# Kernel optimization log

Hardware: AMD Instinct MI355X
Metric: run time of the kernel (lower is better)

The kernel has to match this reference:

```python
import jax, jax.numpy as jnp
import numpy as np

HEADS = 16
EMBED = 1024
HEAD_DIM = EMBED // HEADS


def setup_inputs() -> dict:
    key = jax.random.key(0)
    ks = jax.random.split(key, 7)
    B, S, E = 2, 2048, EMBED
    scale = 1.0 / np.sqrt(E)
    return {
        "query": jax.random.normal(ks[0], (B, S, E), dtype=jnp.float32),
        "key": jax.random.normal(ks[1], (B, S, E), dtype=jnp.float32),
        "value": jax.random.normal(ks[2], (B, S, E), dtype=jnp.float32),
        # nn.Linear(E, E, bias=False) weights, applied as x @ W.T
        "Wq": jax.random.normal(ks[3], (E, E), dtype=jnp.float32) * scale,
        "Wk": jax.random.normal(ks[4], (E, E), dtype=jnp.float32) * scale,
        "Wv": jax.random.normal(ks[5], (E, E), dtype=jnp.float32) * scale,
        "Wo": jax.random.normal(ks[6], (E, E), dtype=jnp.float32) * scale,
    }


def reference(query, key, value, Wq, Wk, Wv, Wo):
    B, S, E = query.shape
    H, D = HEADS, HEAD_DIM

    def split_heads(x, W):
        # [B,S,E] @ W.T -> [B,S,E] -> [B,H,S,D]
        return (x @ W.T).reshape(B, -1, H, D).transpose(0, 2, 1, 3)

    q = split_heads(query, Wq)
    k = split_heads(key, Wk)
    v = split_heads(value, Wv)

    scores = jnp.einsum("bhqd,bhkd->bhqk", q, k) / jnp.sqrt(jnp.float32(D))
    attn = jax.nn.softmax(scores, axis=-1)  # [B,H,S,S]
    x = jnp.einsum("bhqk,bhkd->bhqd", attn, v)
    x = x.transpose(0, 2, 1, 3).reshape(B, -1, H * D)
    return x @ Wo.T
```

## Files before the change

### kernel.cpp

```cpp
#include <hip/hip_runtime.h>
#include <hip/hip_bf16.h>


typedef __attribute__((ext_vector_type(8))) short short8;
typedef __attribute__((ext_vector_type(4))) float f32x4;
typedef __attribute__((ext_vector_type(4))) unsigned short us4;
typedef __attribute__((ext_vector_type(4))) int i32x4;

#define MFMA16(a, b, c) __builtin_amdgcn_mfma_f32_16x16x32_bf16(a, b, c, 0, 0, 0)

static constexpr int B = 2;
static constexpr int S = 2048;
static constexpr int E = 1024;
static constexpr int H = 16;
static constexpr int D = 64;
static constexpr int M = B * S;
static constexpr size_t NE = (size_t)M * E;
static constexpr size_t NW = (size_t)E * E;

static __device__ __forceinline__ unsigned short f2bf(float x) {
  unsigned int u = __float_as_uint(x);
  unsigned int r = (u + 0x7FFFu + ((u >> 16) & 1u)) >> 16;
  return (unsigned short)r;
}

static __device__ __forceinline__ int cvt_pk_bf16(float lo, float hi) {
  int r;
  asm("v_cvt_pk_bf16_f32 %0, %1, %2" : "=v"(r) : "v"(lo), "v"(hi));
  return r;
}

static __device__ __forceinline__ void gload_lds16(const unsigned short* g,
                                                   unsigned short* l) {
  __builtin_amdgcn_global_load_lds(
      (const __attribute__((address_space(1))) unsigned int*)g,
      (__attribute__((address_space(3))) unsigned int*)l, 16, 0, 0);
}

__global__ void cvt_act_kernel(const float* __restrict__ s0,
                               const float* __restrict__ s1,
                               const float* __restrict__ s2,
                               unsigned short* __restrict__ d0,
                               unsigned short* __restrict__ d1,
                               unsigned short* __restrict__ d2, int n4) {
  const float* src = (blockIdx.y == 0) ? s0 : ((blockIdx.y == 1) ? s1 : s2);
  unsigned short* dst = (blockIdx.y == 0) ? d0 : ((blockIdx.y == 1) ? d1 : d2);
  for (int i = blockIdx.x * blockDim.x + threadIdx.x; i < n4;
       i += gridDim.x * blockDim.x) {
    float4 v = reinterpret_cast<const float4*>(src)[i];
    ushort4 o;
    o.x = f2bf(v.x); o.y = f2bf(v.y); o.z = f2bf(v.z); o.w = f2bf(v.w);
    reinterpret_cast<ushort4*>(dst)[i] = o;
  }
}

__global__ void cvt_w_kernel(const float* __restrict__ s0,
                             const float* __restrict__ s1,
                             const float* __restrict__ s2,
                             const float* __restrict__ s3,
                             unsigned short* __restrict__ d0,
                             unsigned short* __restrict__ d1,
                             unsigned short* __restrict__ d2,
                             unsigned short* __restrict__ d3, int n4) {
  const int z = blockIdx.y;
  const float* src = (z == 0) ? s0 : ((z == 1) ? s1 : ((z == 2) ? s2 : s3));
  unsigned short* dst = (z == 0) ? d0 : ((z == 1) ? d1 : ((z == 2) ? d2 : d3));
  for (int i = blockIdx.x * blockDim.x + threadIdx.x; i < n4;
       i += gridDim.x * blockDim.x) {
    float4 v = reinterpret_cast<const float4*>(src)[i];
    ushort4 o;
    o.x = f2bf(v.x); o.y = f2bf(v.y); o.z = f2bf(v.z); o.w = f2bf(v.w);
    reinterpret_cast<ushort4*>(dst)[i] = o;
  }
}

__global__ __launch_bounds__(256) void gemm_proj_kernel(
    const unsigned short* __restrict__ xq, const unsigned short* __restrict__ xk,
    const unsigned short* __restrict__ xv, const unsigned short* __restrict__ wq,
    const unsigned short* __restrict__ wk, const unsigned short* __restrict__ wv,
    unsigned short* __restrict__ Qh, unsigned short* __restrict__ Kh,
    unsigned short* __restrict__ Vt) {
  __shared__ __align__(16) unsigned short As[2][128 * 32];
  __shared__ __align__(16) unsigned short Bs[2][128 * 32];

  const int which = blockIdx.z;
  const unsigned short* A = (which == 0) ? xq : ((which == 1) ? xk : xv);
  const unsigned short* W = (which == 0) ? wq : ((which == 1) ? wk : wv);

  const int wave = threadIdx.x >> 6;
  const int lane = threadIdx.x & 63;
  const int lr = lane & 15;
  const int lk = (lane >> 4) * 8;
  const int m0 = blockIdx.x * 128;
  const int n0 = blockIdx.y * 128;
  const int wm = (wave >> 1) * 64;
  const int wn = (wave & 1) * 64;
  const int srow = lane >> 2;
  const int scol = (lane & 3) * 8;

  f32x4 acc[4][4];
  const f32x4 fz = {0.f, 0.f, 0.f, 0.f};
#pragma unroll
  for (int i = 0; i < 4; ++i)
#pragma unroll
    for (int j = 0; j < 4; ++j) acc[i][j] = fz;

#define STAGE_G(bb, kk)                                                       \
  {                                                                           \
    _Pragma("unroll") for (int i = 0; i < 2; ++i) {                           \
      const int c = wave * 2 + i;                                             \
      const int row = c * 16 + srow;                                          \
      gload_lds16(A + (size_t)(m0 + row) * E + (kk) + scol, &As[bb][c * 512]);\
      gload_lds16(W + (size_t)(n0 + row) * E + (kk) + scol, &Bs[bb][c * 512]);\
    }                                                                         \
  }

  STAGE_G(0, 0);
  __syncthreads();
  int buf = 0;
  for (int kk = 0; kk < E; kk += 32) {
    if (kk + 32 < E) STAGE_G(buf ^ 1, kk + 32);
    short8 af[4], bw[4];
#pragma unroll
    for (int i = 0; i < 4; ++i)
      af[i] = *reinterpret_cast<const short8*>(
          &As[buf][(wm + i * 16 + lr) * 32 + lk]);
#pragma unroll
    for (int j = 0; j < 4; ++j)
      bw[j] = *reinterpret_cast<const short8*>(
          &Bs[buf][(wn + j * 16 + lr) * 32 + lk]);
#pragma unroll
    for (int i = 0; i < 4; ++i)
#pragma unroll
      for (int j = 0; j < 4; ++j) acc[i][j] = MFMA16(af[i], bw[j], acc[i][j]);
    __syncthreads();
    buf ^= 1;
  }
#undef STAGE_G

  const int rbase = (lane >> 4) * 4;
#pragma unroll
  for (int i = 0; i < 4; ++i) {
#pragma unroll
    for (int j = 0; j < 4; ++j) {
      const int col = n0 + wn + j * 16 + lr;
      const int h = col >> 6, d = col & 63;
#pragma unroll
      for (int r = 0; r < 4; ++r) {
        const int row = m0 + wm + i * 16 + rbase + r;
        const int b = row >> 11, s = row & (S - 1);
        const float v = acc[i][j][r];
        if (which == 0) {
          Qh[(((size_t)b * H + h) * S + s) * D + d] = f2bf(v * 0.18033688f);
        } else if (which == 1) {
          Kh[(((size_t)b * H + h) * S + s) * D + d] = f2bf(v);
        } else {
          Vt[(((size_t)b * H + h) * D + d) * S + s] = f2bf(v);
        }
      }
    }
  }
}

__global__ __launch_bounds__(256) void gemm_out_kernel(
    const unsigned short* __restrict__ X, const unsigned short* __restrict__ Wo,
    float* __restrict__ out) {
  __shared__ __align__(16) unsigned short As[2][128 * 32];
  __shared__ __align__(16) unsigned short Bs[2][64 * 32];

  const int wave = threadIdx.x >> 6;
  const int lane = threadIdx.x & 63;
  const int lr = lane & 15;
  const int lk = (lane >> 4) * 8;
  const int m0 = blockIdx.x * 128;
  const int n0 = blockIdx.y * 64;
  const int wm = (wave >> 1) * 64;
  const int wn = (wave & 1) * 32;
  const int srow = lane >> 2;
  const int scol = (lane & 3) * 8;

  f32x4 acc[4][2];
  const f32x4 fz = {0.f, 0.f, 0.f, 0.f};
#pragma unroll
  for (int i = 0; i < 4; ++i)
#pragma unroll
    for (int j = 0; j < 2; ++j) acc[i][j] = fz;

#define STAGE_O(bb, kk)                                                       \
  {                                                                           \
    _Pragma("unroll") for (int i = 0; i < 2; ++i) {                           \
      const int c = wave * 2 + i;                                             \
      const int row = c * 16 + srow;                                          \
      gload_lds16(X + (size_t)(m0 + row) * E + (kk) + scol, &As[bb][c * 512]);\
    }                                                                         \
    gload_lds16(Wo + (size_t)(n0 + wave * 16 + srow) * E + (kk) + scol,       \
                &Bs[bb][wave * 512]);                                         \
  }

  STAGE_O(0, 0);
  __syncthreads();
  int buf = 0;
  for (int kk = 0; kk < E; kk += 32) {
    if (kk + 32 < E) STAGE_O(buf ^ 1, kk + 32);
    short8 af[4], bw[2];
#pragma unroll
    for (int i = 0; i < 4; ++i)
      af[i] = *reinterpret_cast<const short8*>(
          &As[buf][(wm + i * 16 + lr) * 32 + lk]);
#pragma unroll
    for (int j = 0; j < 2; ++j)
      bw[j] = *reinterpret_cast<const short8*>(
          &Bs[buf][(wn + j * 16 + lr) * 32 + lk]);
#pragma unroll
    for (int i = 0; i < 4; ++i)
#pragma unroll
      for (int j = 0; j < 2; ++j) acc[i][j] = MFMA16(af[i], bw[j], acc[i][j]);
    __syncthreads();
    buf ^= 1;
  }
#undef STAGE_O

  const int rbase = (lane >> 4) * 4;
#pragma unroll
  for (int i = 0; i < 4; ++i) {
#pragma unroll
    for (int j = 0; j < 2; ++j) {
      const int col = n0 + wn + j * 16 + lr;
#pragma unroll
      for (int r = 0; r < 4; ++r) {
        const int row = m0 + wm + i * 16 + rbase + r;
        out[(size_t)row * E + col] = acc[i][j][r];
      }
    }
  }
}

__global__ __launch_bounds__(256) void attn_kernel(
    const unsigned short* __restrict__ Qh, const unsigned short* __restrict__ Kh,
    const unsigned short* __restrict__ Vt, unsigned short* __restrict__ Xb) {
  __shared__ __align__(16) unsigned short Ks[2][64 * 64];
  __shared__ __align__(16) unsigned short Vs[2][64 * 64];

  const int wave = threadIdx.x >> 6;
  const int lane = threadIdx.x & 63;
  const int lr = lane & 15;
  const int jj = lane >> 4;
  const int lk = jj * 8;

  const int lin = blockIdx.x + (blockIdx.y << 4);
  const int nlin = (lin & 7) * 64 + (lin >> 3);
  const int qt = nlin & 15;
  const int bh = nlin >> 4;
  const int q0 = qt * 128 + wave * 32;

  const unsigned short* Qp0 = Qh + ((size_t)bh * S + q0) * D;
  const unsigned short* Qp1 = Qp0 + (size_t)16 * D;
  short8 qa0 = *reinterpret_cast<const short8*>(Qp0 + (size_t)lr * D + lk);
  short8 qa1 = *reinterpret_cast<const short8*>(Qp0 + (size_t)lr * D + 32 + lk);
  short8 qb0 = *reinterpret_cast<const short8*>(Qp1 + (size_t)lr * D + lk);
  short8 qb1 = *reinterpret_cast<const short8*>(Qp1 + (size_t)lr * D + 32 + lk);

  const unsigned short* Kbase = Kh + (size_t)bh * S * D;
  const unsigned short* Vbase = Vt + (size_t)bh * D * S;

  const f32x4 fz = {0.f, 0.f, 0.f, 0.f};
  float mrunA = -3.0e38f, lsumA = 0.f;
  float mrunB = -3.0e38f, lsumB = 0.f;
  f32x4 accA[4], accB[4];
#pragma unroll
  for (int dt = 0; dt < 4; ++dt) { accA[dt] = fz; accB[dt] = fz; }

  const int srow = lane >> 3;
  const int sgV = (lane & 7) ^ srow;

#define STAGE_KV(bb, kt)                                                      \
  {                                                                           \
    _Pragma("unroll") for (int i = 0; i < 2; ++i) {                           \
      const int c = wave * 2 + i;                                             \
      const int sgK = (lane & 7) ^ ((srow & 3) | ((c & 1) << 2));             \
      gload_lds16(Kbase + (size_t)((kt) + c * 8 + srow) * D + sgK * 8,        \
                  &Ks[bb][c * 512]);                                          \
      gload_lds16(Vbase + (size_t)(c * 8 + srow) * S + (kt) + sgV * 8,        \
                  &Vs[bb][c * 512]);                                          \
    }                                                                         \
  }

  STAGE_KV(0, 0);
  __syncthreads();
  int buf = 0;

  const int rb = ((lr >> 2) << 3) + (lr & 3);
  const int kswz = (lr & 3) | (((lr >> 2) & 1) << 2);
  const int vswz = lr & 7;

  constexpr int NT = S / 64;
  for (int t = 0; t < NT; ++t) {
    if (t + 1 < NT) STAGE_KV(buf ^ 1, (t + 1) * 64);

    f32x4 sfA[4], sfB[4];
    __builtin_amdgcn_s_setprio(1);
#pragma unroll
    for (int nt = 0; nt < 4; ++nt) {
      const int r = rb + ((nt & 1) << 2) + ((nt >> 1) << 5);
      short8 kf0 = *reinterpret_cast<const short8*>(
          &Ks[buf][r * 64 + ((jj ^ kswz) * 8)]);
      short8 kf1 = *reinterpret_cast<const short8*>(
          &Ks[buf][r * 64 + (((jj + 4) ^ kswz) * 8)]);
      f32x4 za = fz, zb = fz;
      za = MFMA16(kf0, qa0, za);
      za = MFMA16(kf1, qa1, za);
      zb = MFMA16(kf0, qb0, zb);
      zb = MFMA16(kf1, qb1, zb);
      sfA[nt] = za;
      sfB[nt] = zb;
    }
    __builtin_amdgcn_s_setprio(0);

    short8 vf0[4], vf1[4];
#pragma unroll
    for (int dt = 0; dt < 4; ++dt) {
      const int r = dt * 16 + lr;
      vf0[dt] = *reinterpret_cast<const short8*>(
          &Vs[buf][r * 64 + ((jj ^ vswz) * 8)]);
      vf1[dt] = *reinterpret_cast<const short8*>(
          &Vs[buf][r * 64 + (((jj + 4) ^ vswz) * 8)]);
    }

    float mxA = sfA[0][0];
#pragma unroll
    for (int nt = 0; nt < 4; ++nt)
#pragma unroll
      for (int r = 0; r < 4; ++r) mxA = fmaxf(mxA, sfA[nt][r]);
    mxA = fmaxf(mxA, __shfl_xor(mxA, 16));
    mxA = fmaxf(mxA, __shfl_xor(mxA, 32));
    if (__any(mxA > mrunA + 8.f)) {
      const float nm = fmaxf(mrunA, mxA);
      const float fac = __builtin_amdgcn_exp2f(mrunA - nm);
      mrunA = nm;
      lsumA *= fac;
#pragma unroll
      for (int dt = 0; dt < 4; ++dt)
#pragma unroll
        for (int r = 0; r < 4; ++r) accA[dt][r] *= fac;
    }
    float pA[4][4];
#pragma unroll
    for (int nt = 0; nt < 4; ++nt)
#pragma unroll
      for (int r = 0; r < 4; ++r) {
        pA[nt][r] = __builtin_amdgcn_exp2f(sfA[nt][r] - mrunA);
        lsumA += pA[nt][r];
      }
    i32x4 wa0, wa1;
    wa0.x = cvt_pk_bf16(pA[0][0], pA[0][1]);
    wa0.y = cvt_pk_bf16(pA[0][2], pA[0][3]);
    wa0.z = cvt_pk_bf16(pA[1][0], pA[1][1]);
    wa0.w = cvt_pk_bf16(pA[1][2], pA[1][3]);
    wa1.x = cvt_pk_bf16(pA[2][0], pA[2][1]);
    wa1.y = cvt_pk_bf16(pA[2][2], pA[2][3]);
    wa1.z = cvt_pk_bf16(pA[3][0], pA[3][1]);
    wa1.w = cvt_pk_bf16(pA[3][2], pA[3][3]);
    short8 paA0 = __builtin_bit_cast(short8, wa0);
    short8 paA1 = __builtin_bit_cast(short8, wa1);

    float mxB = sfB[0][0];
#pragma unroll
    for (int nt = 0; nt < 4; ++nt)
#pragma unroll
      for (int r = 0; r < 4; ++r) mxB = fmaxf(mxB, sfB[nt][r]);
    mxB = fmaxf(mxB, __shfl_xor(mxB, 16));
    mxB = fmaxf(mxB, __shfl_xor(mxB, 32));
    if (__any(mxB > mrunB + 8.f)) {
      const float nm = fmaxf(mrunB, mxB);
      const float fac = __builtin_amdgcn_exp2f(mrunB - nm);
      mrunB = nm;
      lsumB *= fac;
#pragma unroll
      for (int dt = 0; dt < 4; ++dt)
#pragma unroll
        for (int r = 0; r < 4; ++r) accB[dt][r] *= fac;
    }
    float pB[4][4];
#pragma unroll
    for (int nt = 0; nt < 4; ++nt)
#pragma unroll
      for (int r = 0; r < 4; ++r) {
        pB[nt][r] = __builtin_amdgcn_exp2f(sfB[nt][r] - mrunB);
        lsumB += pB[nt][r];
      }
    i32x4 wb0, wb1;
    wb0.x = cvt_pk_bf16(pB[0][0], pB[0][1]);
    wb0.y = cvt_pk_bf16(pB[0][2], pB[0][3]);
    wb0.z = cvt_pk_bf16(pB[1][0], pB[1][1]);
    wb0.w = cvt_pk_bf16(pB[1][2], pB[1][3]);
    wb1.x = cvt_pk_bf16(pB[2][0], pB[2][1]);
    wb1.y = cvt_pk_bf16(pB[2][2], pB[2][3]);
    wb1.z = cvt_pk_bf16(pB[3][0], pB[3][1]);
    wb1.w = cvt_pk_bf16(pB[3][2], pB[3][3]);
    short8 paB0 = __builtin_bit_cast(short8, wb0);
    short8 paB1 = __builtin_bit_cast(short8, wb1);

    __builtin_amdgcn_s_setprio(1);
#pragma unroll
    for (int dt = 0; dt < 4; ++dt) {
      accA[dt] = MFMA16(vf0[dt], paA0, accA[dt]);
      accA[dt] = MFMA16(vf1[dt], paA1, accA[dt]);
      accB[dt] = MFMA16(vf0[dt], paB0, accB[dt]);
      accB[dt] = MFMA16(vf1[dt], paB1, accB[dt]);
    }
    __builtin_amdgcn_s_setprio(0);

    __syncthreads();
    buf ^= 1;
  }
#undef STAGE_KV

  const int b = bh >> 4, h = bh & (H - 1);
  {
    float ltot = lsumA;
    ltot += __shfl_xor(ltot, 16);
    ltot += __shfl_xor(ltot, 32);
    const float inv = 1.0f / ltot;
    const int row = q0 + lr;
#pragma unroll
    for (int dt = 0; dt < 4; ++dt) {
      us4 o;
#pragma unroll
      for (int r = 0; r < 4; ++r) o[r] = f2bf(accA[dt][r] * inv);
      *reinterpret_cast<us4*>(
          &Xb[((size_t)b * S + row) * E + h * D + dt * 16 + 4 * jj]) = o;
    }
  }
  {
    float ltot = lsumB;
    ltot += __shfl_xor(ltot, 16);
    ltot += __shfl_xor(ltot, 32);
    const float inv = 1.0f / ltot;
    const int row = q0 + 16 + lr;
#pragma unroll
    for (int dt = 0; dt < 4; ++dt) {
      us4 o;
#pragma unroll
      for (int r = 0; r < 4; ++r) o[r] = f2bf(accB[dt][r] * inv);
      *reinterpret_cast<us4*>(
          &Xb[((size_t)b * S + row) * E + h * D + dt * 16 + 4 * jj]) = o;
    }
  }
}

extern "C" void kernel_launch(void* const* d_in, const int* in_sizes, int n_in,
                              void* d_out, int out_size, void* d_ws, size_t ws_size,
                              hipStream_t stream) {
  const float* q_f = (const float*)d_in[0];
  const float* k_f = (const float*)d_in[1];
  const float* v_f = (const float*)d_in[2];
  const float* wq_f = (const float*)d_in[3];
  const float* wk_f = (const float*)d_in[4];
  const float* wv_f = (const float*)d_in[5];
  const float* wo_f = (const float*)d_in[6];

  unsigned short* xq = (unsigned short*)d_ws;
  unsigned short* xk = xq + NE;
  unsigned short* xv = xk + NE;
  unsigned short* wq = xv + NE;
  unsigned short* wk = wq + NW;
  unsigned short* wv = wk + NW;
  unsigned short* wo = wv + NW;
  unsigned short* Qh = wo + NW;
  unsigned short* Kh = Qh + NE;
  unsigned short* Vt = Kh + NE;
  unsigned short* Xb = Vt + NE;

  cvt_act_kernel<<<dim3(512, 3), 256, 0, stream>>>(q_f, k_f, v_f, xq, xk, xv,
                                                   (int)(NE / 4));
  cvt_w_kernel<<<dim3(256, 4), 256, 0, stream>>>(wq_f, wk_f, wv_f, wo_f, wq, wk,
                                                 wv, wo, (int)(NW / 4));

  gemm_proj_kernel<<<dim3(M / 128, E / 128, 3), 256, 0, stream>>>(
      xq, xk, xv, wq, wk, wv, Qh, Kh, Vt);

  attn_kernel<<<dim3(S / 128, B * H), 256, 0, stream>>>(Qh, Kh, Vt, Xb);

  gemm_out_kernel<<<dim3(M / 128, E / 64), 256, 0, stream>>>(Xb, wo,
                                                             (float*)d_out);
}
```

Baseline: 145.4 us.

## Merge conversion kernels, compute softmax row sums via MFMA, incremental KV pointers

Merges the activation and weight fp32-to-bf16 conversion kernels into a single launch so one kernel launch and its tail are avoided. In the attention loop, the per-lane VALU accumulation of exponentials is replaced by MFMA against a vector of bf16 ones, so the row sum comes out already reduced across lanes and the final shuffles are no longer needed. The loop also advances K/V staging pointers incrementally instead of recomputing addresses, and the max reduction is rebalanced into a tree. The row sums now come from bf16-rounded probabilities, which changes numerics slightly, and the extra MFMAs add work to the matrix pipe.

```diff
diff --git a/kernel.cpp b/kernel.cpp
--- a/kernel.cpp
+++ b/kernel.cpp
@@ -37,34 +37,27 @@
       (__attribute__((address_space(3))) unsigned int*)l, 16, 0, 0);
 }
 
-__global__ void cvt_act_kernel(const float* __restrict__ s0,
+__global__ void cvt_all_kernel(const float* __restrict__ s0,
                                const float* __restrict__ s1,
                                const float* __restrict__ s2,
+                               const float* __restrict__ s3,
+                               const float* __restrict__ s4,
+                               const float* __restrict__ s5,
+                               const float* __restrict__ s6,
                                unsigned short* __restrict__ d0,
                                unsigned short* __restrict__ d1,
-                               unsigned short* __restrict__ d2, int n4) {
-  const float* src = (blockIdx.y == 0) ? s0 : ((blockIdx.y == 1) ? s1 : s2);
-  unsigned short* dst = (blockIdx.y == 0) ? d0 : ((blockIdx.y == 1) ? d1 : d2);
-  for (int i = blockIdx.x * blockDim.x + threadIdx.x; i < n4;
-       i += gridDim.x * blockDim.x) {
-    float4 v = reinterpret_cast<const float4*>(src)[i];
-    ushort4 o;
-    o.x = f2bf(v.x); o.y = f2bf(v.y); o.z = f2bf(v.z); o.w = f2bf(v.w);
-    reinterpret_cast<ushort4*>(dst)[i] = o;
-  }
-}
-
-__global__ void cvt_w_kernel(const float* __restrict__ s0,
-                             const float* __restrict__ s1,
-                             const float* __restrict__ s2,
-                             const float* __restrict__ s3,
-                             unsigned short* __restrict__ d0,
-                             unsigned short* __restrict__ d1,
-                             unsigned short* __restrict__ d2,
-                             unsigned short* __restrict__ d3, int n4) {
+                               unsigned short* __restrict__ d2,
+                               unsigned short* __restrict__ d3,
+                               unsigned short* __restrict__ d4,
+                               unsigned short* __restrict__ d5,
+                               unsigned short* __restrict__ d6, int nAct4,
+                               int nW4) {
   const int z = blockIdx.y;
-  const float* src = (z == 0) ? s0 : ((z == 1) ? s1 : ((z == 2) ? s2 : s3));
-  unsigned short* dst = (z == 0) ? d0 : ((z == 1) ? d1 : ((z == 2) ? d2 : d3));
+  const float* srcs[7] = {s0, s1, s2, s3, s4, s5, s6};
+  unsigned short* dsts[7] = {d0, d1, d2, d3, d4, d5, d6};
+  const float* src = srcs[z];
+  unsigned short* dst = dsts[z];
+  const int n4 = (z < 3) ? nAct4 : nW4;
   for (int i = blockIdx.x * blockDim.x + threadIdx.x; i < n4;
        i += gridDim.x * blockDim.x) {
     float4 v = reinterpret_cast<const float4*>(src)[i];
@@ -264,28 +257,39 @@
   const unsigned short* Vbase = Vt + (size_t)bh * D * S;
 
   const f32x4 fz = {0.f, 0.f, 0.f, 0.f};
-  float mrunA = -3.0e38f, lsumA = 0.f;
-  float mrunB = -3.0e38f, lsumB = 0.f;
-  f32x4 accA[4], accB[4];
+  const short8 ones = {(short)0x3F80, (short)0x3F80, (short)0x3F80,
+                       (short)0x3F80, (short)0x3F80, (short)0x3F80,
+                       (short)0x3F80, (short)0x3F80};
+  float mrunA = -3.0e38f, mrunB = -3.0e38f;
+  f32x4 accA[4], accB[4], laccA = fz, laccB = fz;
 #pragma unroll
   for (int dt = 0; dt < 4; ++dt) { accA[dt] = fz; accB[dt] = fz; }
 
   const int srow = lane >> 3;
   const int sgV = (lane & 7) ^ srow;
 
-#define STAGE_KV(bb, kt)                                                      \
+  const unsigned short* kptr[2];
+  const unsigned short* vptr[2];
+#pragma unroll
+  for (int i = 0; i < 2; ++i) {
+    const int c = wave * 2 + i;
+    const int sgK = (lane & 7) ^ ((srow & 3) | ((c & 1) << 2));
+    kptr[i] = Kbase + (size_t)(c * 8 + srow) * D + sgK * 8;
+    vptr[i] = Vbase + (size_t)(c * 8 + srow) * S + sgV * 8;
+  }
+
+#define STAGE_KV(bb)                                                          \
   {                                                                           \
     _Pragma("unroll") for (int i = 0; i < 2; ++i) {                           \
       const int c = wave * 2 + i;                                             \
-      const int sgK = (lane & 7) ^ ((srow & 3) | ((c & 1) << 2));             \
-      gload_lds16(Kbase + (size_t)((kt) + c * 8 + srow) * D + sgK * 8,        \
-                  &Ks[bb][c * 512]);                                          \
-      gload_lds16(Vbase + (size_t)(c * 8 + srow) * S + (kt) + sgV * 8,        \
-                  &Vs[bb][c * 512]);                                          \
+      gload_lds16(kptr[i], &Ks[bb][c * 512]);                                 \
+      gload_lds16(vptr[i], &Vs[bb][c * 512]);                                 \
+      kptr[i] += 64 * D;                                                      \
+      vptr[i] += 64;                                                          \
     }                                                                         \
   }
 
-  STAGE_KV(0, 0);
+  STAGE_KV(0);
   __syncthreads();
   int buf = 0;
 
@@ -295,7 +299,7 @@
 
   constexpr int NT = S / 64;
   for (int t = 0; t < NT; ++t) {
-    if (t + 1 < NT) STAGE_KV(buf ^ 1, (t + 1) * 64);
+    if (t + 1 < NT) STAGE_KV(buf ^ 1);
 
     f32x4 sfA[4], sfB[4];
     __builtin_amdgcn_s_setprio(1);
@@ -326,79 +330,75 @@
           &Vs[buf][r * 64 + (((jj + 4) ^ vswz) * 8)]);
     }
 
-    float mxA = sfA[0][0];
+    float tA[4];
 #pragma unroll
     for (int nt = 0; nt < 4; ++nt)
-#pragma unroll
-      for (int r = 0; r < 4; ++r) mxA = fmaxf(mxA, sfA[nt][r]);
+      tA[nt] = fmaxf(fmaxf(sfA[nt][0], sfA[nt][1]),
+                     fmaxf(sfA[nt][2], sfA[nt][3]));
+    float mxA = fmaxf(fmaxf(tA[0], tA[1]), fmaxf(tA[2], tA[3]));
     mxA = fmaxf(mxA, __shfl_xor(mxA, 16));
     mxA = fmaxf(mxA, __shfl_xor(mxA, 32));
     if (__any(mxA > mrunA + 8.f)) {
       const float nm = fmaxf(mrunA, mxA);
       const float fac = __builtin_amdgcn_exp2f(mrunA - nm);
       mrunA = nm;
-      lsumA *= fac;
+      laccA *= fac;
 #pragma unroll
       for (int dt = 0; dt < 4; ++dt)
 #pragma unroll
         for (int r = 0; r < 4; ++r) accA[dt][r] *= fac;
     }
-    float pA[4][4];
 #pragma unroll
     for (int nt = 0; nt < 4; ++nt)
 #pragma unroll
-      for (int r = 0; r < 4; ++r) {
-        pA[nt][r] = __builtin_amdgcn_exp2f(sfA[nt][r] - mrunA);
-        lsumA += pA[nt][r];
-      }
+      for (int r = 0; r < 4; ++r)
+        sfA[nt][r] = __builtin_amdgcn_exp2f(sfA[nt][r] - mrunA);
     i32x4 wa0, wa1;
-    wa0.x = cvt_pk_bf16(pA[0][0], pA[0][1]);
-    wa0.y = cvt_pk_bf16(pA[0][2], pA[0][3]);
-    wa0.z = cvt_pk_bf16(pA[1][0], pA[1][1]);
-    wa0.w = cvt_pk_bf16(pA[1][2], pA[1][3]);
-    wa1.x = cvt_pk_bf16(pA[2][0], pA[2][1]);
-    wa1.y = cvt_pk_bf16(pA[2][2], pA[2][3]);
-    wa1.z = cvt_pk_bf16(pA[3][0], pA[3][1]);
-    wa1.w = cvt_pk_bf16(pA[3][2], pA[3][3]);
-    short8 paA0 = __builtin_bit_cast(short8, wa0);
-    short8 paA1 = __builtin_bit_cast(short8, wa1);
-
-    float mxB = sfB[0][0];
+    wa0.x = cvt_pk_bf16(sfA[0][0], sfA[0][1]);
+    wa0.y = cvt_pk_bf16(sfA[0][2], sfA[0][3]);
+    wa0.z = cvt_pk_bf16(sfA[1][0], sfA[1][1]);
+    wa0.w = cvt_pk_bf16(sfA[1][2], sfA[1][3]);
+    wa1.x = cvt_pk_bf16(sfA[2][0], sfA[2][1]);
+    wa1.y = cvt_pk_bf16(sfA[2][2], sfA[2][3]);
+    wa1.z = cvt_pk_bf16(sfA[3][0], sfA[3][1]);
+    wa1.w = cvt_pk_bf16(sfA[3][2], sfA[3][3]);
+    const short8 paA0 = __builtin_bit_cast(short8, wa0);
+    const short8 paA1 = __builtin_bit_cast(short8, wa1);
+
+    float tB[4];
 #pragma unroll
     for (int nt = 0; nt < 4; ++nt)
-#pragma unroll
-      for (int r = 0; r < 4; ++r) mxB = fmaxf(mxB, sfB[nt][r]);
+      tB[nt] = fmaxf(fmaxf(sfB[nt][0], sfB[nt][1]),
+                     fmaxf(sfB[nt][2], sfB[nt][3]));
+    float mxB = fmaxf(fmaxf(tB[0], tB[1]), fmaxf(tB[2], tB[3]));
     mxB = fmaxf(mxB, __shfl_xor(mxB, 16));
     mxB = fmaxf(mxB, __shfl_xor(mxB, 32));
     if (__any(mxB > mrunB + 8.f)) {
       const float nm = fmaxf(mrunB, mxB);
       const float fac = __builtin_amdgcn_exp2f(mrunB - nm);
       mrunB = nm;
-      lsumB *= fac;
+      laccB *= fac;
 #pragma unroll
       for (int dt = 0; dt < 4; ++dt)
 #pragma unroll
         for (int r = 0; r < 4; ++r) accB[dt][r] *= fac;
     }
-    float pB[4][4];
 #pragma unroll
     for (int nt = 0; nt < 4; ++nt)
 #pragma unroll
-      for (int r = 0; r < 4; ++r) {
-        pB[nt][r] = __builtin_amdgcn_exp2f(sfB[nt][r] - mrunB);
-        lsumB += pB[nt][r];
-      }
+      for (int r = 0; r < 4; ++r)
+        sfB[nt][r] = __builtin_amdgcn_exp2f(sfB[nt][r] - mrunB);
     i32x4 wb0, wb1;
-    wb0.x = cvt_pk_bf16(pB[0][0], pB[0][1]);
-    wb0.y = cvt_pk_bf16(pB[0][2], pB[0][3]);
-    wb0.z = cvt_pk_bf16(pB[1][0], pB[1][1]);
-    wb0.w = cvt_pk_bf16(pB[1][2], pB[1][3]);
-    wb1.x = cvt_pk_bf16(pB[2][0], pB[2][1]);
-    wb1.y = cvt_pk_bf16(pB[2][2], pB[2][3]);
-    wb1.z = cvt_pk_bf16(pB[3][0], pB[3][1]);
-    wb1.w = cvt_pk_bf16(pB[3][2], pB[3][3]);
-    short8 paB0 = __builtin_bit_cast(short8, wb0);
-    short8 paB1 = __builtin_bit_cast(short8, wb1);
+    wb0.x = cvt_pk_bf16(sfB[0][0], sfB[0][1]);
+    wb0.y = cvt_pk_bf16(sfB[0][2], sfB[0][3]);
+    wb0.z = cvt_pk_bf16(sfB[1][0], sfB[1][1]);
+    wb0.w = cvt_pk_bf16(sfB[1][2], sfB[1][3]);
+    wb1.x = cvt_pk_bf16(sfB[2][0], sfB[2][1]);
+    wb1.y = cvt_pk_bf16(sfB[2][2], sfB[2][3]);
+    wb1.z = cvt_pk_bf16(sfB[3][0], sfB[3][1]);
+    wb1.w = cvt_pk_bf16(sfB[3][2], sfB[3][3]);
+    const short8 paB0 = __builtin_bit_cast(short8, wb0);
+    const short8 paB1 = __builtin_bit_cast(short8, wb1);
 
     __builtin_amdgcn_s_setprio(1);
 #pragma unroll
@@ -408,6 +408,10 @@
       accB[dt] = MFMA16(vf0[dt], paB0, accB[dt]);
       accB[dt] = MFMA16(vf1[dt], paB1, accB[dt]);
     }
+    laccA = MFMA16(ones, paA0, laccA);
+    laccA = MFMA16(ones, paA1, laccA);
+    laccB = MFMA16(ones, paB0, laccB);
+    laccB = MFMA16(ones, paB1, laccB);
     __builtin_amdgcn_s_setprio(0);
 
     __syncthreads();
@@ -417,10 +421,7 @@
 
   const int b = bh >> 4, h = bh & (H - 1);
   {
-    float ltot = lsumA;
-    ltot += __shfl_xor(ltot, 16);
-    ltot += __shfl_xor(ltot, 32);
-    const float inv = 1.0f / ltot;
+    const float inv = 1.0f / laccA[0];
     const int row = q0 + lr;
 #pragma unroll
     for (int dt = 0; dt < 4; ++dt) {
@@ -432,10 +433,7 @@
     }
   }
   {
-    float ltot = lsumB;
-    ltot += __shfl_xor(ltot, 16);
-    ltot += __shfl_xor(ltot, 32);
-    const float inv = 1.0f / ltot;
+    const float inv = 1.0f / laccB[0];
     const int row = q0 + 16 + lr;
 #pragma unroll
     for (int dt = 0; dt < 4; ++dt) {
@@ -471,10 +469,9 @@
   unsigned short* Vt = Kh + NE;
   unsigned short* Xb = Vt + NE;
 
-  cvt_act_kernel<<<dim3(512, 3), 256, 0, stream>>>(q_f, k_f, v_f, xq, xk, xv,
-                                                   (int)(NE / 4));
-  cvt_w_kernel<<<dim3(256, 4), 256, 0, stream>>>(wq_f, wk_f, wv_f, wo_f, wq, wk,
-                                                 wv, wo, (int)(NW / 4));
+  cvt_all_kernel<<<dim3(512, 7), 256, 0, stream>>>(
+      q_f, k_f, v_f, wq_f, wk_f, wv_f, wo_f, xq, xk, xv, wq, wk, wv, wo,
+      (int)(NE / 4), (int)(NW / 4));
 
   gemm_proj_kernel<<<dim3(M / 128, E / 128, 3), 256, 0, stream>>>(
       xq, xk, xv, wq, wk, wv, Qh, Kh, Vt);
```

Result: no change. 143.7 us (median of 2 runs) (-1.1%).
